# Performance work log

Hardware: AMD Instinct MI355X
Metric: run time of the kernel (lower is better)

Reference implementation:

```python
import jax, jax.numpy as jnp
import numpy as np

B, S, D = 8, 2048, 512


def setup_inputs() -> dict:
    key = jax.random.key(0)
    ks = jax.random.split(key, 11)
    scale = 1.0 / np.sqrt(D)
    inp = {"x": jax.random.normal(ks[0], (B, S, D), dtype=jnp.float32)}
    names = ["q", "k", "v", "g", "o"]
    for i, n in enumerate(names):
        inp[f"W{n}"] = jax.random.normal(ks[1 + 2 * i], (D, D), dtype=jnp.float32) * scale
        inp[f"b{n}"] = jax.random.normal(ks[2 + 2 * i], (D,), dtype=jnp.float32) * 0.01
    return inp


def reference(x, Wq, bq, Wk, bk, Wv, bv, Wg, bg, Wo, bo):
    # Projections (torch nn.Linear: x @ W.T + b)
    Q = x @ Wq.T + bq            # (B,S,D)
    K = x @ Wk.T + bk
    V = x @ Wv.T + bv
    gamma = jax.nn.sigmoid(x @ Wg.T + bg)

    # Recurrent linear-attention scan over time.
    # State St: (B,D,D); update: St = gamma_t[:, :, None] * St + k_t ⊗ v_t
    # (decay broadcasts along the key/row dimension, matching
    #  gamma_i.transpose(1,2) * S in the torch code)
    def step(St, qkvg):
        q_t, k_t, v_t, g_t = qkvg           # each (B,D)
        St = g_t[:, :, None] * St + k_t[:, :, None] * v_t[:, None, :]
        out_t = jnp.einsum('bd,bde->be', q_t, St)  # q_i @ S
        return St, out_t

    S0 = jnp.zeros((B, D, D), dtype=x.dtype)
    # time-major inputs for scan: (S,B,D)
    seq = (Q.transpose(1, 0, 2), K.transpose(1, 0, 2),
           V.transpose(1, 0, 2), gamma.transpose(1, 0, 2))
    _, outs = jax.lax.scan(step, S0, seq)   # outs: (S,B,D)
    O = outs.transpose(1, 0, 2)             # (B,S,D)
    return O @ Wo.T + bo
```

## Files before the change

### kernel.cpp

```cpp
#include <hip/hip_runtime.h>
#include <hip/hip_bf16.h>
#include <stdint.h>


#define B_ 8
#define S_ 2048
#define D_ 512
#define M_ (B_ * S_)
#define NSUB 64
#define SUBL 32
#define NSUP 8
#define SUPL 256

typedef __bf16 bf16x8 __attribute__((ext_vector_type(8)));
typedef float f32x4 __attribute__((ext_vector_type(4)));

__device__ __forceinline__ float bflo(uint32_t u){ return __uint_as_float(u<<16); }
__device__ __forceinline__ float bfhi(uint32_t u){ return __uint_as_float(u&0xffff0000u); }
__device__ __forceinline__ uint16_t f2bf(float f){
    uint32_t u = __float_as_uint(f);
    return (uint16_t)((u + 0x7fffu + ((u>>16)&1u)) >> 16);
}
__device__ __forceinline__ uint32_t pack2bf(float a, float b){
    return (uint32_t)f2bf(a) | ((uint32_t)f2bf(b)<<16);
}
__device__ __forceinline__ void gload16(const void* g, void* l){
    __builtin_amdgcn_global_load_lds(
        (const __attribute__((address_space(1))) uint32_t*)g,
        (__attribute__((address_space(3))) uint32_t*)l, 16, 0, 0);
}

__global__ __launch_bounds__(256) void conv_x(const float* __restrict__ in,
                                              uint16_t* __restrict__ out){
    const size_t i = ((size_t)blockIdx.x*256 + threadIdx.x)*8;
    float4 a = *(const float4*)&in[i];
    float4 b = *(const float4*)&in[i+4];
    uint4 o; o.x=pack2bf(a.x,a.y); o.y=pack2bf(a.z,a.w); o.z=pack2bf(b.x,b.y); o.w=pack2bf(b.z,b.w);
    *(uint4*)&out[i] = o;
}
__global__ __launch_bounds__(256) void conv_w(const float* w0, const float* w1, const float* w2,
                                              const float* w3, const float* w4,
                                              uint16_t* __restrict__ out){
    const float* ws[5] = {w0,w1,w2,w3,w4};
    const float* in = ws[blockIdx.y];
    uint16_t* o = out + (size_t)blockIdx.y*D_*D_;
    const size_t i = ((size_t)blockIdx.x*256 + threadIdx.x)*8;
    float4 a = *(const float4*)&in[i];
    float4 b = *(const float4*)&in[i+4];
    uint4 u; u.x=pack2bf(a.x,a.y); u.y=pack2bf(a.z,a.w); u.z=pack2bf(b.x,b.y); u.w=pack2bf(b.z,b.w);
    *(uint4*)&o[i] = u;
}

__global__ __launch_bounds__(256) void proj4(const uint16_t* __restrict__ A,
                                             const uint16_t* __restrict__ Wb,
                                             const float* __restrict__ bq_,
                                             const float* __restrict__ bk_,
                                             const float* __restrict__ bv_,
                                             const float* __restrict__ bg_,
                                             uint16_t* __restrict__ Qb,
                                             uint16_t* __restrict__ Kb,
                                             uint16_t* __restrict__ VT,
                                             uint16_t* __restrict__ Gb)
{
    __shared__ __attribute__((aligned(16))) uint16_t SM[2][16384];
    const int tid = threadIdx.x, wave = tid>>6, lane = tid&63;
    const int m0 = blockIdx.x*128, n0 = blockIdx.y*128;
    const int wr = (wave>>1)*64, wc = (wave&1)*64;
    const int fr = lane&15, fq = lane>>4;
    const int sect = blockIdx.y >> 2;
    const int n0c = n0 & 511;
    f32x4 acc[4][4] = {};

    auto STAGE = [&](int kt, int p){
        const int k0 = kt*64;
#pragma unroll
        for (int i = 0; i < 4; ++i) {
            const int c = i*256 + tid;
            const int row = c>>3, kc = ((c&7) ^ (row&7))*8;
            const int ldsb = (i*256 + wave*64)*8;
            gload16(&A [(size_t)(m0+row)*D_ + k0 + kc], &SM[p][ldsb]);
            gload16(&Wb[(size_t)(n0+row)*D_ + k0 + kc], &SM[p][8192+ldsb]);
        }
    };
    auto COMP = [&](int p){
#pragma unroll
        for (int kk = 0; kk < 64; kk += 32) {
            const int sc = (kk + fq*8) ^ ((fr&7)<<3);
            bf16x8 af[4], bfv[4];
#pragma unroll
            for (int m = 0; m < 4; ++m) af[m]  = *(const bf16x8*)&SM[p][(wr+m*16+fr)*64 + sc];
#pragma unroll
            for (int n = 0; n < 4; ++n) bfv[n] = *(const bf16x8*)&SM[p][8192+(wc+n*16+fr)*64 + sc];
            if (sect == 2) {
#pragma unroll
                for (int m = 0; m < 4; ++m)
#pragma unroll
                    for (int n = 0; n < 4; ++n)
                        acc[m][n] = __builtin_amdgcn_mfma_f32_16x16x32_bf16(bfv[n], af[m], acc[m][n], 0,0,0);
            } else {
#pragma unroll
                for (int m = 0; m < 4; ++m)
#pragma unroll
                    for (int n = 0; n < 4; ++n)
                        acc[m][n] = __builtin_amdgcn_mfma_f32_16x16x32_bf16(af[m], bfv[n], acc[m][n], 0,0,0);
            }
        }
    };

    STAGE(0, 0);
    __syncthreads();
    int p = 0;
    for (int kt = 0; kt < 8; ++kt) {
        if (kt < 7) STAGE(kt+1, p^1);
        COMP(p);
        __syncthreads();
        p ^= 1;
    }

    uint16_t (*L)[136] = (uint16_t(*)[136])&SM[0][0];
    const float* bias = (sect==0) ? bq_ : (sect==1) ? bk_ : (sect==2) ? bv_ : bg_;
    if (sect == 2) {
#pragma unroll
        for (int n = 0; n < 4; ++n)
#pragma unroll
            for (int q = 0; q < 4; ++q) {
                const int dvl = wc + n*16 + fq*4 + q;
                const float bvv = bias[n0c + dvl];
#pragma unroll
                for (int m = 0; m < 4; ++m)
                    L[dvl][wr + m*16 + fr] = f2bf(acc[m][n][q] + bvv);
            }
    } else {
#pragma unroll
        for (int n = 0; n < 4; ++n) {
            const int cl = wc + n*16 + fr;
            const float bvv = bias[n0c + cl];
#pragma unroll
            for (int m = 0; m < 4; ++m)
#pragma unroll
                for (int q = 0; q < 4; ++q) {
                    float c = acc[m][n][q] + bvv;
                    if (sect == 3) c = 1.f/(1.f + expf(-c));
                    L[wr + m*16 + fq*4 + q][cl] = f2bf(c);
                }
        }
    }
    __syncthreads();
    const int bb = m0 >> 11, t0 = m0 & 2047;
#pragma unroll
    for (int it = 0; it < 8; ++it) {
        const int r = it*16 + (tid>>4), c8 = (tid&15)*8;
        uint4 v = *(uint4*)&L[r][c8];
        if (sect == 0)      *(uint4*)&Qb[(size_t)(m0+r)*D_ + n0c + c8] = v;
        else if (sect == 1) *(uint4*)&Kb[(size_t)(m0+r)*D_ + n0c + c8] = v;
        else if (sect == 3) *(uint4*)&Gb[(size_t)(m0+r)*D_ + n0c + c8] = v;
        else                *(uint4*)&VT[((size_t)bb*D_ + n0c + r)*S_ + t0 + c8] = v;
    }
}

__global__ __launch_bounds__(256) void mfma_gemm(const uint16_t* __restrict__ A,
                                                 const uint16_t* __restrict__ Wt,
                                                 const float* __restrict__ bias,
                                                 float* __restrict__ out)
{
    __shared__ __attribute__((aligned(16))) uint16_t SM[2][16384];
    const int tid = threadIdx.x, wave = tid>>6, lane = tid&63;
    const int m0 = blockIdx.x*128, n0 = blockIdx.y*128;
    const int wr = (wave>>1)*64, wc = (wave&1)*64;
    const int fr = lane&15, fq = lane>>4;
    f32x4 acc[4][4] = {};

    auto STAGE = [&](int kt, int p){
        const int k0 = kt*64;
#pragma unroll
        for (int i = 0; i < 4; ++i) {
            const int c = i*256 + tid;
            const int row = c>>3, kc = ((c&7) ^ (row&7))*8;
            const int ldsb = (i*256 + wave*64)*8;
            gload16(&A [(size_t)(m0+row)*D_ + k0 + kc], &SM[p][ldsb]);
            gload16(&Wt[(size_t)(n0+row)*D_ + k0 + kc], &SM[p][8192+ldsb]);
        }
    };
    auto COMP = [&](int p){
#pragma unroll
        for (int kk = 0; kk < 64; kk += 32) {
            const int sc = (kk + fq*8) ^ ((fr&7)<<3);
            bf16x8 af[4], bfv[4];
#pragma unroll
            for (int m = 0; m < 4; ++m) af[m]  = *(const bf16x8*)&SM[p][(wr+m*16+fr)*64 + sc];
#pragma unroll
            for (int n = 0; n < 4; ++n) bfv[n] = *(const bf16x8*)&SM[p][8192+(wc+n*16+fr)*64 + sc];
#pragma unroll
            for (int m = 0; m < 4; ++m)
#pragma unroll
                for (int n = 0; n < 4; ++n)
                    acc[m][n] = __builtin_amdgcn_mfma_f32_16x16x32_bf16(af[m], bfv[n], acc[m][n], 0,0,0);
        }
    };

    STAGE(0, 0);
    __syncthreads();
    int p = 0;
    for (int kt = 0; kt < 8; ++kt) {
        if (kt < 7) STAGE(kt+1, p^1);
        COMP(p);
        __syncthreads();
        p ^= 1;
    }

    float (*L32)[68] = (float(*)[68])&SM[0][0];
#pragma unroll
    for (int h = 0; h < 2; ++h) {
        if (wc == h*64) {
#pragma unroll
            for (int n = 0; n < 4; ++n) {
                const float bvv = bias[n0 + wc + n*16 + fr];
#pragma unroll
                for (int m = 0; m < 4; ++m)
#pragma unroll
                    for (int q = 0; q < 4; ++q)
                        L32[wr + m*16 + fq*4 + q][n*16 + fr] = acc[m][n][q] + bvv;
            }
        }
        __syncthreads();
#pragma unroll
        for (int it = 0; it < 8; ++it) {
            const int r = it*16 + (tid>>4), c4 = (tid&15)*4;
            *(uint4*)&out[(size_t)(m0+r)*D_ + n0 + h*64 + c4] = *(uint4*)&L32[r][c4];
        }
        __syncthreads();
    }
}

__global__ __launch_bounds__(256) void prep(const uint16_t* __restrict__ Gb,
                                            uint16_t* __restrict__ Qb,
                                            uint16_t* __restrict__ Kb,
                                            uint16_t* __restrict__ KT,
                                            float* __restrict__ T)
{
    const int sub = blockIdx.x, b = blockIdx.y;
    const int tid = threadIdx.x;
    const int dk0 = tid*2;
    const size_t rowbase = ((size_t)b*S_ + sub*SUBL)*D_;
    const uint16_t* gp = Gb + rowbase + dk0;
    uint16_t*       qp = Qb + rowbase + dk0;
    uint16_t*       kp = Kb + rowbase + dk0;

    float mu0 = 1.f, mu1 = 1.f;
    uint32_t ksave[SUBL];
#pragma unroll
    for (int t = 0; t < SUBL; ++t) {
        const uint32_t g2 = *(const uint32_t*)(gp + (size_t)t*D_);
        const uint32_t qu = *(const uint32_t*)(qp + (size_t)t*D_);
        const uint32_t ku = *(const uint32_t*)(kp + (size_t)t*D_);
        mu0 = fmaxf(mu0*bflo(g2), 1e-30f);
        mu1 = fmaxf(mu1*bfhi(g2), 1e-30f);
        const float r0 = __builtin_amdgcn_rcpf(mu0);
        const float r1 = __builtin_amdgcn_rcpf(mu1);
        *(uint32_t*)(qp + (size_t)t*D_) = pack2bf(bflo(qu)*mu0, bfhi(qu)*mu1);
        const uint32_t kw = pack2bf(bflo(ku)*r0, bfhi(ku)*r1);
        *(uint32_t*)(kp + (size_t)t*D_) = kw;
        ksave[t] = kw;
    }
    T[((size_t)b*NSUB + sub)*D_ + dk0]     = mu0;
    T[((size_t)b*NSUB + sub)*D_ + dk0 + 1] = mu1;

    uint16_t* d0 = &KT[((size_t)b*D_ + dk0)*S_ + sub*SUBL];
    uint16_t* d1 = d0 + S_;
#pragma unroll
    for (int q4 = 0; q4 < 4; ++q4) {
        uint4 lo, hi;
        lo.x = (ksave[q4*8+0]&0xffffu) | (ksave[q4*8+1]<<16);
        lo.y = (ksave[q4*8+2]&0xffffu) | (ksave[q4*8+3]<<16);
        lo.z = (ksave[q4*8+4]&0xffffu) | (ksave[q4*8+5]<<16);
        lo.w = (ksave[q4*8+6]&0xffffu) | (ksave[q4*8+7]<<16);
        hi.x = (ksave[q4*8+0]>>16) | (ksave[q4*8+1]&0xffff0000u);
        hi.y = (ksave[q4*8+2]>>16) | (ksave[q4*8+3]&0xffff0000u);
        hi.z = (ksave[q4*8+4]>>16) | (ksave[q4*8+5]&0xffff0000u);
        hi.w = (ksave[q4*8+6]>>16) | (ksave[q4*8+7]&0xffff0000u);
        *(uint4*)&d0[q4*8] = lo;
        *(uint4*)&d1[q4*8] = hi;
    }
}

__global__ __launch_bounds__(512) void tables(const float* __restrict__ T,
                                              float* __restrict__ Pre,
                                              float* __restrict__ Suf,
                                              float* __restrict__ Lam)
{
    const int sp = blockIdx.x, b = blockIdx.y, dk = threadIdx.x;
    float run = 1.f;
#pragma unroll
    for (int m = 0; m < 8; ++m) {
        Pre[((size_t)b*NSUB + sp*8+m)*D_ + dk] = run;
        run *= T[((size_t)b*NSUB + sp*8+m)*D_ + dk];
    }
    Lam[((size_t)b*NSUP + sp)*D_ + dk] = run;
    float rs = 1.f;
#pragma unroll
    for (int m = 7; m >= 0; --m) {
        rs *= T[((size_t)b*NSUB + sp*8+m)*D_ + dk];
        Suf[((size_t)b*NSUB + sp*8+m)*D_ + dk] = rs;
    }
}

__device__ __forceinline__ int swz(int r, int c){ return r*D_ + (c ^ ((r&7)<<3)); }

__global__ __launch_bounds__(256) void pairsA(const uint16_t* __restrict__ Qt,
                                              const uint16_t* __restrict__ Kh,
                                              const float* __restrict__ T,
                                              uint16_t* __restrict__ P)
{
    __shared__ __attribute__((aligned(16))) uint16_t qs[SUBL*D_];
    __shared__ __attribute__((aligned(16))) uint16_t ks[SUBL*D_];
    __shared__ float D_lds[D_];
    const int idx = blockIdx.x, sp = blockIdx.y, b = blockIdx.z;
    int i = 0;
    while (((i+1)*(i+2))/2 <= idx) ++i;
    const int j = idx - (i*(i+1))/2;

    const int tid = threadIdx.x, wave = tid>>6, lane = tid&63;
    const int fr = lane&15, fq = lane>>4;
    const int mq = wave>>1, nq = wave&1;
    const size_t qrow = (size_t)b*S_ + sp*SUPL + i*SUBL;
    const size_t krow = (size_t)b*S_ + sp*SUPL + j*SUBL;
    const size_t prow = ((size_t)(b*NSUP + sp)*SUPL + i*SUBL);

#pragma unroll
    for (int z = 0; z < 8; ++z) {
        int ch = z*256 + tid, r = ch>>6, c = (ch&63)*8;
        *(uint4*)&qs[swz(r,c)] = *(const uint4*)&Qt[(qrow + r)*D_ + c];
    }
    const int dkA = tid*2, dkB = tid*2+1;
    float d0 = 1.f, d1 = 1.f;
    for (int m = j; m < i; ++m) {
        d0 *= T[((size_t)b*NSUB + sp*8 + m)*D_ + dkA];
        d1 *= T[((size_t)b*NSUB + sp*8 + m)*D_ + dkB];
    }
    D_lds[dkA] = d0; D_lds[dkB] = d1;
    __syncthreads();

#pragma unroll
    for (int z = 0; z < 8; ++z) {
        int ch = z*256 + tid, r = ch>>6, c = (ch&63)*8;
        uint4 u = *(const uint4*)&Kh[(krow + r)*D_ + c];
        uint4 o;
        o.x = pack2bf(bflo(u.x)*D_lds[c+0], bfhi(u.x)*D_lds[c+1]);
        o.y = pack2bf(bflo(u.y)*D_lds[c+2], bfhi(u.y)*D_lds[c+3]);
        o.z = pack2bf(bflo(u.z)*D_lds[c+4], bfhi(u.z)*D_lds[c+5]);
        o.w = pack2bf(bflo(u.w)*D_lds[c+6], bfhi(u.w)*D_lds[c+7]);
        *(uint4*)&ks[swz(r,c)] = o;
    }
    __syncthreads();

    f32x4 a0 = {}, a1 = {}, a2 = {}, a3 = {};
#pragma unroll
    for (int kk = 0; kk < 512; kk += 128) {
        bf16x8 q0 = *(const bf16x8*)&qs[swz(mq*16+fr, kk      + fq*8)];
        bf16x8 k0 = *(const bf16x8*)&ks[swz(nq*16+fr, kk      + fq*8)];
        bf16x8 q1 = *(const bf16x8*)&qs[swz(mq*16+fr, kk + 32 + fq*8)];
        bf16x8 k1 = *(const bf16x8*)&ks[swz(nq*16+fr, kk + 32 + fq*8)];
        bf16x8 q2 = *(const bf16x8*)&qs[swz(mq*16+fr, kk + 64 + fq*8)];
        bf16x8 k2 = *(const bf16x8*)&ks[swz(nq*16+fr, kk + 64 + fq*8)];
        bf16x8 q3 = *(const bf16x8*)&qs[swz(mq*16+fr, kk + 96 + fq*8)];
        bf16x8 k3 = *(const bf16x8*)&ks[swz(nq*16+fr, kk + 96 + fq*8)];
        a0 = __builtin_amdgcn_mfma_f32_16x16x32_bf16(q0, k0, a0, 0,0,0);
        a1 = __builtin_amdgcn_mfma_f32_16x16x32_bf16(q1, k1, a1, 0,0,0);
        a2 = __builtin_amdgcn_mfma_f32_16x16x32_bf16(q2, k2, a2, 0,0,0);
        a3 = __builtin_amdgcn_mfma_f32_16x16x32_bf16(q3, k3, a3, 0,0,0);
    }
    const int ul = nq*16 + fr;
#pragma unroll
    for (int q_ = 0; q_ < 4; ++q_) {
        const int tl = mq*16 + fq*4 + q_;
        float v = a0[q_] + a1[q_] + a2[q_] + a3[q_];
        if (i == j && ul > tl) v = 0.f;
        P[(prow + tl)*SUPL + j*SUBL + ul] = f2bf(v);
    }
}

__global__ __launch_bounds__(256) void dsgemm(const uint16_t* __restrict__ VT,
                                              const uint16_t* __restrict__ KT,
                                              const float* __restrict__ Suf,
                                              uint16_t* __restrict__ Sst)
{
    __shared__ __attribute__((aligned(16))) uint16_t As[2][128][40];
    __shared__ __attribute__((aligned(16))) uint16_t Bs[2][128][40];
    const int tile = blockIdx.x, c = blockIdx.y, b = blockIdx.z;
    const int m0 = (tile&3)*128, n0 = (tile>>2)*128;
    const int tid = threadIdx.x, wave = tid>>6, lane = tid&63;
    const int wr = (wave>>1)*64, wc = (wave&1)*64;
    const int fr = lane&15, fq = lane>>4;
    f32x4 acc[4][4] = {};

    auto STAGE = [&](int j, int p){
        const int t0 = c*SUPL + j*SUBL;
#pragma unroll
        for (int ch = tid; ch < 512; ch += 256) {
            int row = ch>>2, tc = (ch&3)*8;
            *(uint4*)&As[p][row][tc] = *(const uint4*)&VT[((size_t)b*D_ + m0+row)*S_ + t0 + tc];
        }
#pragma unroll
        for (int ch = tid; ch < 512; ch += 256) {
            int row = ch>>2, tc = (ch&3)*8;
            uint4 u = *(const uint4*)&KT[((size_t)b*D_ + n0+row)*S_ + t0 + tc];
            float sf = Suf[((size_t)b*NSUB + c*8 + j)*D_ + n0 + row];
            uint4 o;
            o.x = pack2bf(bflo(u.x)*sf, bfhi(u.x)*sf);
            o.y = pack2bf(bflo(u.y)*sf, bfhi(u.y)*sf);
            o.z = pack2bf(bflo(u.z)*sf, bfhi(u.z)*sf);
            o.w = pack2bf(bflo(u.w)*sf, bfhi(u.w)*sf);
            *(uint4*)&Bs[p][row][tc] = o;
        }
    };

    STAGE(0, 0);
    __syncthreads();
    int p = 0;
    for (int j = 0; j < 8; ++j) {
        if (j < 7) STAGE(j+1, p^1);
        bf16x8 af[4], bf[4];
#pragma unroll
        for (int m = 0; m < 4; ++m) af[m] = *(const bf16x8*)&As[p][wr+m*16+fr][fq*8];
#pragma unroll
        for (int n = 0; n < 4; ++n) bf[n] = *(const bf16x8*)&Bs[p][wc+n*16+fr][fq*8];
#pragma unroll
        for (int m = 0; m < 4; ++m)
#pragma unroll
            for (int n = 0; n < 4; ++n)
                acc[m][n] = __builtin_amdgcn_mfma_f32_16x16x32_bf16(af[m], bf[n], acc[m][n], 0,0,0);
        __syncthreads();
        p ^= 1;
    }
#pragma unroll
    for (int n = 0; n < 4; ++n) {
        const int dk = n0 + wc + n*16 + fr;
#pragma unroll
        for (int m = 0; m < 4; ++m)
#pragma unroll
            for (int q = 0; q < 4; ++q) {
                const int dv = m0 + wr + m*16 + fq*4 + q;
                Sst[(((size_t)c*B_ + b)*D_ + dv)*D_ + dk] = f2bf(acc[m][n][q]);
            }
    }
}

__global__ __launch_bounds__(256) void scanfix(uint16_t* __restrict__ Sst,
                                               const float* __restrict__ Lam)
{
    const int id = blockIdx.x*256 + threadIdx.x;
    const int g = id & 63, dv = (id>>6) & 511, b = id >> 15;
    const int dk = g*8;
    float s[8];
    {
        uint4 u = *(const uint4*)&Sst[(((size_t)0*B_ + b)*D_ + dv)*D_ + dk];
        s[0]=bflo(u.x); s[1]=bfhi(u.x); s[2]=bflo(u.y); s[3]=bfhi(u.y);
        s[4]=bflo(u.z); s[5]=bfhi(u.z); s[6]=bflo(u.w); s[7]=bfhi(u.w);
    }
    for (int c = 1; c < 7; ++c) {
        const size_t bs = (((size_t)c*B_ + b)*D_ + dv)*D_ + dk;
        uint4 d = *(const uint4*)&Sst[bs];
        float4 l0 = *(const float4*)&Lam[((size_t)b*NSUP + c)*D_ + dk];
        float4 l1 = *(const float4*)&Lam[((size_t)b*NSUP + c)*D_ + dk + 4];
        s[0] = l0.x*s[0] + bflo(d.x); s[1] = l0.y*s[1] + bfhi(d.x);
        s[2] = l0.z*s[2] + bflo(d.y); s[3] = l0.w*s[3] + bfhi(d.y);
        s[4] = l1.x*s[4] + bflo(d.z); s[5] = l1.y*s[5] + bfhi(d.z);
        s[6] = l1.z*s[6] + bflo(d.w); s[7] = l1.w*s[7] + bfhi(d.w);
        uint4 o;
        o.x = pack2bf(s[0],s[1]); o.y = pack2bf(s[2],s[3]);
        o.z = pack2bf(s[4],s[5]); o.w = pack2bf(s[6],s[7]);
        *(uint4*)&Sst[bs] = o;
    }
}

__global__ __launch_bounds__(256) void bigout(const uint16_t* __restrict__ Qt,
                                              const float* __restrict__ Pre,
                                              const uint16_t* __restrict__ Sst,
                                              const uint16_t* __restrict__ Pb,
                                              const uint16_t* __restrict__ VT,
                                              uint16_t* __restrict__ O)
{
    __shared__ __attribute__((aligned(16))) uint16_t SM[2][16384];
    __shared__ float PreL[4*512];
    const int m0 = blockIdx.x*128, n0 = blockIdx.y*128;
    const int b = blockIdx.z>>3, sp = blockIdx.z&7;
    const int tid = threadIdx.x, wave = tid>>6, lane = tid&63;
    const int wr = (wave>>1)*64, wc = (wave&1)*64;
    const int fr = lane&15, fq = lane>>4;
    const int i0 = m0>>5;

#pragma unroll
    for (int z = 0; z < 8; ++z) {
        int idx = z*256 + tid;
        PreL[idx] = Pre[((size_t)b*NSUB + sp*8 + i0 + (idx>>9))*D_ + (idx&511)];
    }
    f32x4 acc[4][4] = {};
    uint4 areg[4];

    auto ISSUE_A = [&](int kt){
        const int k0 = kt*64;
#pragma unroll
        for (int z = 0; z < 4; ++z) {
            int ch = z*256 + tid, r = ch>>3, cc = (ch&7)*8;
            areg[z] = *(const uint4*)&Qt[((size_t)b*S_ + sp*SUPL + m0 + r)*D_ + k0 + cc];
        }
    };
    auto WRITE_A = [&](int kt, int p){
        const int k0 = kt*64;
#pragma unroll
        for (int z = 0; z < 4; ++z) {
            int ch = z*256 + tid, r = ch>>3, cc = (ch&7)*8;
            const float* pr = &PreL[((r>>5)<<9) + k0 + cc];
            uint4 u = areg[z];
            uint4 o;
            o.x = pack2bf(bflo(u.x)*pr[0], bfhi(u.x)*pr[1]);
            o.y = pack2bf(bflo(u.y)*pr[2], bfhi(u.y)*pr[3]);
            o.z = pack2bf(bflo(u.z)*pr[4], bfhi(u.z)*pr[5]);
            o.w = pack2bf(bflo(u.w)*pr[6], bfhi(u.w)*pr[7]);
            *(uint4*)&SM[p][r*64 + (cc ^ ((r&7)<<3))] = o;
        }
    };
    auto STAGE_A_GL = [&](int kt, int p){
        const int u0 = (kt-8)*64;
#pragma unroll
        for (int z = 0; z < 4; ++z) {
            int ch = z*256 + tid, row = ch>>3, kc = ((ch&7) ^ (row&7))*8;
            int ldsb = (z*256 + wave*64)*8;
            gload16(&Pb[((size_t)(b*NSUP + sp)*SUPL + m0 + row)*SUPL + u0 + kc], &SM[p][ldsb]);
        }
    };
    auto STAGE_B = [&](int kt, int p){
        if (kt < 8) {
            const int k0 = kt*64;
#pragma unroll
            for (int z = 0; z < 4; ++z) {
                int ch = z*256 + tid, row = ch>>3, kc = ((ch&7) ^ (row&7))*8;
                int ldsb = (z*256 + wave*64)*8;
                gload16(&Sst[(((size_t)(sp-1)*B_ + b)*D_ + n0 + row)*D_ + k0 + kc], &SM[p][8192+ldsb]);
            }
        } else {
            const int u0 = (kt-8)*64;
#pragma unroll
            for (int z = 0; z < 4; ++z) {
                int ch = z*256 + tid, row = ch>>3, kc = ((ch&7) ^ (row&7))*8;
                int ldsb = (z*256 + wave*64)*8;
                gload16(&VT[((size_t)b*D_ + n0 + row)*S_ + sp*SUPL + u0 + kc], &SM[p][8192+ldsb]);
            }
        }
    };
    auto COMP = [&](int p, int kt){
        const bf16x8 zz = {};
#pragma unroll
        for (int kk = 0; kk < 64; kk += 32) {
            const int sc = (kk + fq*8) ^ ((fr&7)<<3);
            bf16x8 af[4], bfv[4];
#pragma unroll
            for (int m = 0; m < 4; ++m) af[m] = *(const bf16x8*)&SM[p][(wr+m*16+fr)*64 + sc];
            if (kt >= 8) {
                const int jb = ((kt-8)*64 + kk) >> 5;
#pragma unroll
                for (int m = 0; m < 4; ++m) {
                    const int ib = (m0 + wr + m*16) >> 5;
                    if (jb > ib) af[m] = zz;
                }
            }
#pragma unroll
            for (int n = 0; n < 4; ++n) bfv[n] = *(const bf16x8*)&SM[p][8192+(wc+n*16+fr)*64 + sc];
#pragma unroll
            for (int m = 0; m < 4; ++m)
#pragma unroll
                for (int n = 0; n < 4; ++n)
                    acc[m][n] = __builtin_amdgcn_mfma_f32_16x16x32_bf16(af[m], bfv[n], acc[m][n], 0,0,0);
        }
    };

    const int kt0 = (sp == 0) ? 8 : 0;
    if (kt0 < 8) {
        ISSUE_A(kt0);
        STAGE_B(kt0, 0);
        __syncthreads();
        WRITE_A(kt0, 0);
    } else {
        STAGE_A_GL(kt0, 0);
        STAGE_B(kt0, 0);
    }
    __syncthreads();

    int p = 0;
    for (int kt = kt0; kt < 12; ++kt) {
        const int nxt = kt + 1;
        if (nxt < 12) {
            if (nxt < 8) ISSUE_A(nxt); else STAGE_A_GL(nxt, p^1);
            STAGE_B(nxt, p^1);
        }
        COMP(p, kt);
        if (nxt < 12 && nxt < 8) WRITE_A(nxt, p^1);
        __syncthreads();
        p ^= 1;
    }

    uint16_t (*L)[136] = (uint16_t(*)[136])&SM[0][0];
#pragma unroll
    for (int n = 0; n < 4; ++n) {
        const int cl = wc + n*16 + fr;
#pragma unroll
        for (int m = 0; m < 4; ++m)
#pragma unroll
            for (int q = 0; q < 4; ++q)
                L[wr + m*16 + fq*4 + q][cl] = f2bf(acc[m][n][q]);
    }
    __syncthreads();
#pragma unroll
    for (int it = 0; it < 8; ++it) {
        const int r = it*16 + (tid>>4), c8 = (tid&15)*8;
        *(uint4*)&O[((size_t)b*S_ + sp*SUPL + m0 + r)*D_ + n0 + c8] = *(uint4*)&L[r][c8];
    }
}

extern "C" void kernel_launch(void* const* d_in, const int* in_sizes, int n_in,
                              void* d_out, int out_size, void* d_ws, size_t ws_size,
                              hipStream_t stream)
{
    (void)in_sizes; (void)n_in; (void)out_size; (void)ws_size;
    const float* x  = (const float*)d_in[0];
    const float* Wq = (const float*)d_in[1];  const float* bq = (const float*)d_in[2];
    const float* Wk = (const float*)d_in[3];  const float* bk = (const float*)d_in[4];
    const float* Wv = (const float*)d_in[5];  const float* bv = (const float*)d_in[6];
    const float* Wg = (const float*)d_in[7];  const float* bg = (const float*)d_in[8];
    const float* Wo = (const float*)d_in[9];  const float* bo = (const float*)d_in[10];

    char* w = (char*)d_ws;
    const size_t MD2 = (size_t)M_*D_*2;
    uint16_t* Wb = (uint16_t*)w;                       w += 5*(size_t)D_*D_*2;
    uint16_t* xb = (uint16_t*)w;                       w += MD2;
    uint16_t* Qb = (uint16_t*)w;                       w += MD2;
    uint16_t* Kb = (uint16_t*)w;                       w += MD2;
    uint16_t* KT = (uint16_t*)w;                       w += MD2;
    uint16_t* VT = (uint16_t*)w;                       w += MD2;
    uint16_t* Gb = (uint16_t*)w;                       w += MD2;
    uint16_t* Sst = (uint16_t*)w;                      w += (size_t)7*B_*D_*D_*2;
    uint16_t* Pb  = (uint16_t*)w;                      w += (size_t)B_*NSUP*SUPL*SUPL*2;
    float*    T   = (float*)w;                         w += (size_t)B_*NSUB*D_*4;
    float*    Pre = (float*)w;                         w += (size_t)B_*NSUB*D_*4;
    float*    Suf = (float*)w;                         w += (size_t)B_*NSUB*D_*4;
    float*    Lam = (float*)w;                         w += (size_t)B_*NSUP*D_*4;

    conv_x<<<dim3(M_*D_/2048), 256, 0, stream>>>(x, xb);
    conv_w<<<dim3(D_*D_/2048, 5), 256, 0, stream>>>(Wq, Wk, Wv, Wg, Wo, Wb);

    proj4<<<dim3(M_/128, 16), 256, 0, stream>>>(xb, Wb, bq, bk, bv, bg, Qb, Kb, VT, Gb);

    prep<<<dim3(NSUB, B_), 256, 0, stream>>>(Gb, Qb, Kb, KT, T);
    tables<<<dim3(NSUP, B_), 512, 0, stream>>>(T, Pre, Suf, Lam);

    pairsA<<<dim3(36, NSUP, B_), 256, 0, stream>>>(Qb, Kb, T, Pb);
    dsgemm<<<dim3(16, 7, B_), 256, 0, stream>>>(VT, KT, Suf, Sst);
    scanfix<<<dim3(1024), 256, 0, stream>>>(Sst, Lam);

    bigout<<<dim3(2, 4, B_*NSUP), 256, 0, stream>>>(Qb, Pre, Sst, Pb, VT, xb);

    mfma_gemm<<<dim3(M_/128, D_/128), 256, 0, stream>>>(xb, Wb + 4*(size_t)D_*D_, bo, (float*)d_out);
}
```

Before: 201.9 us.

## Retile projection GEMM to 256x256 blocks with 4-stage pipeline and swizzled grid

The fused Q/K/V/G projection kernel moves from 128x128 tiles with double buffering to 256x256 tiles on 512 threads. It uses a 4-deep LDS pipeline with explicit vmcnt waits, raised wave priority during MFMA work, and a half-by-half epilogue. The output GEMM also gets a 1D grid with a block swizzle for better L2 locality. Larger tiles and deeper prefetch aim to raise arithmetic intensity and hide load latency, at the cost of higher register and LDS pressure, which may lower occupancy.

```diff
diff --git a/kernel.cpp b/kernel.cpp
--- a/kernel.cpp
+++ b/kernel.cpp
@@ -51,110 +51,140 @@
     *(uint4*)&o[i] = u;
 }
 
-__global__ __launch_bounds__(256) void proj4(const uint16_t* __restrict__ A,
-                                             const uint16_t* __restrict__ Wb,
-                                             const float* __restrict__ bq_,
-                                             const float* __restrict__ bk_,
-                                             const float* __restrict__ bv_,
-                                             const float* __restrict__ bg_,
-                                             uint16_t* __restrict__ Qb,
-                                             uint16_t* __restrict__ Kb,
-                                             uint16_t* __restrict__ VT,
-                                             uint16_t* __restrict__ Gb)
-{
-    __shared__ __attribute__((aligned(16))) uint16_t SM[2][16384];
+__global__ __launch_bounds__(512, 2) void proj4(const uint16_t* __restrict__ A,
+                                                const uint16_t* __restrict__ Wb,
+                                                const float* __restrict__ bq_,
+                                                const float* __restrict__ bk_,
+                                                const float* __restrict__ bv_,
+                                                const float* __restrict__ bg_,
+                                                uint16_t* __restrict__ Qb,
+                                                uint16_t* __restrict__ Kb,
+                                                uint16_t* __restrict__ VT,
+                                                uint16_t* __restrict__ Gb)
+{
+    __shared__ __attribute__((aligned(16))) uint16_t SM[65536];
+    const int id  = blockIdx.x;
+    const int bx  = id & 63, by = id >> 6;
     const int tid = threadIdx.x, wave = tid>>6, lane = tid&63;
-    const int m0 = blockIdx.x*128, n0 = blockIdx.y*128;
-    const int wr = (wave>>1)*64, wc = (wave&1)*64;
-    const int fr = lane&15, fq = lane>>4;
-    const int sect = blockIdx.y >> 2;
-    const int n0c = n0 & 511;
-    f32x4 acc[4][4] = {};
-
-    auto STAGE = [&](int kt, int p){
-        const int k0 = kt*64;
-#pragma unroll
-        for (int i = 0; i < 4; ++i) {
-            const int c = i*256 + tid;
-            const int row = c>>3, kc = ((c&7) ^ (row&7))*8;
-            const int ldsb = (i*256 + wave*64)*8;
-            gload16(&A [(size_t)(m0+row)*D_ + k0 + kc], &SM[p][ldsb]);
-            gload16(&Wb[(size_t)(n0+row)*D_ + k0 + kc], &SM[p][8192+ldsb]);
-        }
-    };
-    auto COMP = [&](int p){
-#pragma unroll
-        for (int kk = 0; kk < 64; kk += 32) {
-            const int sc = (kk + fq*8) ^ ((fr&7)<<3);
-            bf16x8 af[4], bfv[4];
-#pragma unroll
-            for (int m = 0; m < 4; ++m) af[m]  = *(const bf16x8*)&SM[p][(wr+m*16+fr)*64 + sc];
-#pragma unroll
-            for (int n = 0; n < 4; ++n) bfv[n] = *(const bf16x8*)&SM[p][8192+(wc+n*16+fr)*64 + sc];
-            if (sect == 2) {
-#pragma unroll
-                for (int m = 0; m < 4; ++m)
-#pragma unroll
-                    for (int n = 0; n < 4; ++n)
-                        acc[m][n] = __builtin_amdgcn_mfma_f32_16x16x32_bf16(bfv[n], af[m], acc[m][n], 0,0,0);
-            } else {
-#pragma unroll
-                for (int m = 0; m < 4; ++m)
-#pragma unroll
-                    for (int n = 0; n < 4; ++n)
-                        acc[m][n] = __builtin_amdgcn_mfma_f32_16x16x32_bf16(af[m], bfv[n], acc[m][n], 0,0,0);
-            }
-        }
-    };
-
-    STAGE(0, 0);
-    __syncthreads();
-    int p = 0;
-    for (int kt = 0; kt < 8; ++kt) {
-        if (kt < 7) STAGE(kt+1, p^1);
-        COMP(p);
-        __syncthreads();
-        p ^= 1;
-    }
-
-    uint16_t (*L)[136] = (uint16_t(*)[136])&SM[0][0];
+    const int m0  = bx*256, n0 = by*256;
+    const int wm  = wave>>2, wn = wave&3;
+    const int fr  = lane&15, fq = lane>>4;
+    const int sect = by >> 1;
+    const int n0c  = (by&1)*256;
+    const int sx   = (fr ^ (fr>>2)) & 3;
+    const int col  = (fq ^ sx) * 8;
+
+    f32x4 acc[8][4] = {};
+
+    auto STAGE = [&](int ct, int s){
+        const int base = s*16384;
+#pragma unroll
+        for (int z = 0; z < 2; ++z) {
+            const int ch  = z*512 + tid;
+            const int row = ch >> 2, sl = ch & 3;
+            const int kc  = (sl ^ ((row ^ (row>>2)) & 3)) * 8;
+            const int ldsb = base + (z*512 + wave*64)*8;
+            gload16(&A [(size_t)(m0+row)*D_ + ct*32 + kc], &SM[ldsb]);
+            gload16(&Wb[(size_t)(n0+row)*D_ + ct*32 + kc], &SM[ldsb + 8192]);
+        }
+    };
+
+    STAGE(0, 0); STAGE(1, 1); STAGE(2, 2);
+#pragma unroll
+    for (int i = 0; i < 16; ++i) {
+        const int s = i & 3;
+        if (i < 13) STAGE(i+3, (i+3)&3);
+        __builtin_amdgcn_sched_barrier(0);
+        if      (i < 13) asm volatile("s_waitcnt vmcnt(12)" ::: "memory");
+        else if (i == 13) asm volatile("s_waitcnt vmcnt(8)"  ::: "memory");
+        else if (i == 14) asm volatile("s_waitcnt vmcnt(4)"  ::: "memory");
+        else              asm volatile("s_waitcnt vmcnt(0)"  ::: "memory");
+        __builtin_amdgcn_s_barrier();
+        __builtin_amdgcn_sched_barrier(0);
+
+        const int ab = s*16384;
+        bf16x8 af[8], bfv[4];
+#pragma unroll
+        for (int mf = 0; mf < 8; ++mf)
+            af[mf] = *(const bf16x8*)&SM[ab + (wm*128 + mf*16 + fr)*32 + col];
+#pragma unroll
+        for (int nf = 0; nf < 4; ++nf)
+            bfv[nf] = *(const bf16x8*)&SM[ab + 8192 + (wn*64 + nf*16 + fr)*32 + col];
+
+        __builtin_amdgcn_s_setprio(1);
+        if (sect == 2) {
+#pragma unroll
+            for (int nf = 0; nf < 4; ++nf)
+#pragma unroll
+                for (int mf = 0; mf < 8; ++mf)
+                    acc[mf][nf] = __builtin_amdgcn_mfma_f32_16x16x32_bf16(bfv[nf], af[mf], acc[mf][nf], 0,0,0);
+        } else {
+#pragma unroll
+            for (int nf = 0; nf < 4; ++nf)
+#pragma unroll
+                for (int mf = 0; mf < 8; ++mf)
+                    acc[mf][nf] = __builtin_amdgcn_mfma_f32_16x16x32_bf16(af[mf], bfv[nf], acc[mf][nf], 0,0,0);
+        }
+        __builtin_amdgcn_s_setprio(0);
+        __builtin_amdgcn_sched_barrier(0);
+        __builtin_amdgcn_s_barrier();
+        __builtin_amdgcn_sched_barrier(0);
+    }
+
     const float* bias = (sect==0) ? bq_ : (sect==1) ? bk_ : (sect==2) ? bv_ : bg_;
     if (sect == 2) {
-#pragma unroll
-        for (int n = 0; n < 4; ++n)
-#pragma unroll
-            for (int q = 0; q < 4; ++q) {
-                const int dvl = wc + n*16 + fq*4 + q;
-                const float bvv = bias[n0c + dvl];
-#pragma unroll
-                for (int m = 0; m < 4; ++m)
-                    L[dvl][wr + m*16 + fr] = f2bf(acc[m][n][q] + bvv);
+        uint16_t (*Lv)[132] = (uint16_t(*)[132])SM;
+        const int bb = m0 >> 11, t0 = m0 & 2047;
+#pragma unroll
+        for (int h = 0; h < 2; ++h) {
+            if (wm == h) {
+#pragma unroll
+                for (int nf = 0; nf < 4; ++nf)
+#pragma unroll
+                    for (int q = 0; q < 4; ++q) {
+                        const int dv = wn*64 + nf*16 + fq*4 + q;
+                        const float bvv = bias[n0c + dv];
+#pragma unroll
+                        for (int mf = 0; mf < 8; ++mf)
+                            Lv[dv][mf*16 + fr] = f2bf(acc[mf][nf][q] + bvv);
+                    }
             }
+            __syncthreads();
+            const int r = tid>>1, c0 = (tid&1)*64;
+#pragma unroll
+            for (int e = 0; e < 8; ++e)
+                *(uint4*)&VT[((size_t)bb*D_ + n0c + r)*S_ + t0 + h*128 + c0 + e*8] =
+                    *(uint4*)&Lv[r][c0 + e*8];
+            __syncthreads();
+        }
     } else {
-#pragma unroll
-        for (int n = 0; n < 4; ++n) {
-            const int cl = wc + n*16 + fr;
-            const float bvv = bias[n0c + cl];
-#pragma unroll
-            for (int m = 0; m < 4; ++m)
-#pragma unroll
-                for (int q = 0; q < 4; ++q) {
-                    float c = acc[m][n][q] + bvv;
-                    if (sect == 3) c = 1.f/(1.f + expf(-c));
-                    L[wr + m*16 + fq*4 + q][cl] = f2bf(c);
+        uint16_t (*L)[264] = (uint16_t(*)[264])SM;
+        uint16_t* dst = (sect==0) ? Qb : (sect==1) ? Kb : Gb;
+#pragma unroll
+        for (int h = 0; h < 2; ++h) {
+            if (wm == h) {
+#pragma unroll
+                for (int nf = 0; nf < 4; ++nf) {
+                    const int cl = wn*64 + nf*16 + fr;
+                    const float bvv = bias[n0c + cl];
+#pragma unroll
+                    for (int mf = 0; mf < 8; ++mf)
+#pragma unroll
+                        for (int q = 0; q < 4; ++q) {
+                            float c = acc[mf][nf][q] + bvv;
+                            if (sect == 3) c = 1.f/(1.f + expf(-c));
+                            L[mf*16 + fq*4 + q][cl] = f2bf(c);
+                        }
                 }
-        }
-    }
-    __syncthreads();
-    const int bb = m0 >> 11, t0 = m0 & 2047;
-#pragma unroll
-    for (int it = 0; it < 8; ++it) {
-        const int r = it*16 + (tid>>4), c8 = (tid&15)*8;
-        uint4 v = *(uint4*)&L[r][c8];
-        if (sect == 0)      *(uint4*)&Qb[(size_t)(m0+r)*D_ + n0c + c8] = v;
-        else if (sect == 1) *(uint4*)&Kb[(size_t)(m0+r)*D_ + n0c + c8] = v;
-        else if (sect == 3) *(uint4*)&Gb[(size_t)(m0+r)*D_ + n0c + c8] = v;
-        else                *(uint4*)&VT[((size_t)bb*D_ + n0c + r)*S_ + t0 + c8] = v;
+            }
+            __syncthreads();
+            const int r = tid>>2, c0 = (tid&3)*64;
+#pragma unroll
+            for (int e = 0; e < 8; ++e)
+                *(uint4*)&dst[(size_t)(m0 + h*128 + r)*D_ + n0c + c0 + e*8] =
+                    *(uint4*)&L[r][c0 + e*8];
+            __syncthreads();
+        }
     }
 }
 
@@ -164,8 +194,11 @@
                                                  float* __restrict__ out)
 {
     __shared__ __attribute__((aligned(16))) uint16_t SM[2][16384];
+    const int id = blockIdx.x;
+    const int bx = (id & 7) + 8*((id >> 3) & 15);
+    const int by = id >> 7;
     const int tid = threadIdx.x, wave = tid>>6, lane = tid&63;
-    const int m0 = blockIdx.x*128, n0 = blockIdx.y*128;
+    const int m0 = bx*128, n0 = by*128;
     const int wr = (wave>>1)*64, wc = (wave&1)*64;
     const int fr = lane&15, fq = lane>>4;
     f32x4 acc[4][4] = {};
@@ -648,7 +681,7 @@
     conv_x<<<dim3(M_*D_/2048), 256, 0, stream>>>(x, xb);
     conv_w<<<dim3(D_*D_/2048, 5), 256, 0, stream>>>(Wq, Wk, Wv, Wg, Wo, Wb);
 
-    proj4<<<dim3(M_/128, 16), 256, 0, stream>>>(xb, Wb, bq, bk, bv, bg, Qb, Kb, VT, Gb);
+    proj4<<<dim3(512), 512, 0, stream>>>(xb, Wb, bq, bk, bv, bg, Qb, Kb, VT, Gb);
 
     prep<<<dim3(NSUB, B_), 256, 0, stream>>>(Gb, Qb, Kb, KT, T);
     tables<<<dim3(NSUP, B_), 512, 0, stream>>>(T, Pre, Suf, Lam);
@@ -659,5 +692,5 @@
 
     bigout<<<dim3(2, 4, B_*NSUP), 256, 0, stream>>>(Qb, Pre, Sst, Pb, VT, xb);
 
-    mfma_gemm<<<dim3(M_/128, D_/128), 256, 0, stream>>>(xb, Wb + 4*(size_t)D_*D_, bo, (float*)d_out);
-}
+    mfma_gemm<<<dim3(512), 256, 0, stream>>>(xb, Wb + 4*(size_t)D_*D_, bo, (float*)d_out);
+}
```

After: 424.3 us. +110.1%, slower.

## Fuse x fp32-to-bf16 conversion into projection GEMM and remap block order

Applied to the files above, without the earlier changes.

Removes the separate conv_x kernel. proj4 now loads fp32 x directly into registers, converts it to bf16 and writes it into swizzled LDS, overlapping the next tile's global loads with the current MFMA compute. Both GEMMs switch to a 1D grid with a grouped block-index remap so that consecutive blocks share row tiles, aiming at better cache reuse. The fused path reads x in fp32 once per column tile (16 times) instead of reading bf16 copies, which adds global traffic and register pressure in exchange for dropping a full pass over x.

```diff
diff --git a/kernel.cpp b/kernel.cpp
--- a/kernel.cpp
+++ b/kernel.cpp
@@ -30,14 +30,6 @@
         (__attribute__((address_space(3))) uint32_t*)l, 16, 0, 0);
 }
 
-__global__ __launch_bounds__(256) void conv_x(const float* __restrict__ in,
-                                              uint16_t* __restrict__ out){
-    const size_t i = ((size_t)blockIdx.x*256 + threadIdx.x)*8;
-    float4 a = *(const float4*)&in[i];
-    float4 b = *(const float4*)&in[i+4];
-    uint4 o; o.x=pack2bf(a.x,a.y); o.y=pack2bf(a.z,a.w); o.z=pack2bf(b.x,b.y); o.w=pack2bf(b.z,b.w);
-    *(uint4*)&out[i] = o;
-}
 __global__ __launch_bounds__(256) void conv_w(const float* w0, const float* w1, const float* w2,
                                               const float* w3, const float* w4,
                                               uint16_t* __restrict__ out){
@@ -51,7 +43,7 @@
     *(uint4*)&o[i] = u;
 }
 
-__global__ __launch_bounds__(256) void proj4(const uint16_t* __restrict__ A,
+__global__ __launch_bounds__(256) void proj4(const float* __restrict__ X,
                                              const uint16_t* __restrict__ Wb,
                                              const float* __restrict__ bq_,
                                              const float* __restrict__ bk_,
@@ -63,22 +55,47 @@
                                              uint16_t* __restrict__ Gb)
 {
     __shared__ __attribute__((aligned(16))) uint16_t SM[2][16384];
+    const int id = blockIdx.x;
+    const int bx = (id & 7) + 8*((id >> 3) & 15);
+    const int by = id >> 7;
     const int tid = threadIdx.x, wave = tid>>6, lane = tid&63;
-    const int m0 = blockIdx.x*128, n0 = blockIdx.y*128;
+    const int m0 = bx*128, n0 = by*128;
     const int wr = (wave>>1)*64, wc = (wave&1)*64;
     const int fr = lane&15, fq = lane>>4;
-    const int sect = blockIdx.y >> 2;
+    const int sect = by >> 2;
     const int n0c = n0 & 511;
     f32x4 acc[4][4] = {};
-
-    auto STAGE = [&](int kt, int p){
+    float4 areg[4][2];
+
+    auto ISSUE_A = [&](int kt){
+        const int k0 = kt*64;
+#pragma unroll
+        for (int z = 0; z < 4; ++z) {
+            const int c = z*256 + tid, row = c>>3, cc = (c&7)*8;
+            const float* src = &X[(size_t)(m0+row)*D_ + k0 + cc];
+            areg[z][0] = *(const float4*)src;
+            areg[z][1] = *(const float4*)(src + 4);
+        }
+    };
+    auto WRITE_A = [&](int p){
+#pragma unroll
+        for (int z = 0; z < 4; ++z) {
+            const int c = z*256 + tid, row = c>>3, cc = (c&7)*8;
+            uint4 o;
+            o.x = pack2bf(areg[z][0].x, areg[z][0].y);
+            o.y = pack2bf(areg[z][0].z, areg[z][0].w);
+            o.z = pack2bf(areg[z][1].x, areg[z][1].y);
+            o.w = pack2bf(areg[z][1].z, areg[z][1].w);
+            *(uint4*)&SM[p][row*64 + (cc ^ ((row&7)<<3))] = o;
+        }
+    };
+    auto STAGE_B = [&](int kt, int p){
         const int k0 = kt*64;
 #pragma unroll
         for (int i = 0; i < 4; ++i) {
             const int c = i*256 + tid;
             const int row = c>>3, kc = ((c&7) ^ (row&7))*8;
             const int ldsb = (i*256 + wave*64)*8;
-            gload16(&A [(size_t)(m0+row)*D_ + k0 + kc], &SM[p][ldsb]);
             gload16(&Wb[(size_t)(n0+row)*D_ + k0 + kc], &SM[p][8192+ldsb]);
         }
     };
@@ -107,12 +124,14 @@
         }
     };
 
-    STAGE(0, 0);
+    ISSUE_A(0); STAGE_B(0, 0); WRITE_A(0);
     __syncthreads();
     int p = 0;
     for (int kt = 0; kt < 8; ++kt) {
-        if (kt < 7) STAGE(kt+1, p^1);
+        const int nxt = kt + 1;
+        if (nxt < 8) { ISSUE_A(nxt); STAGE_B(nxt, p^1); }
         COMP(p);
+        if (nxt < 8) WRITE_A(p^1);
         __syncthreads();
         p ^= 1;
     }
@@ -164,8 +183,11 @@
                                                  float* __restrict__ out)
 {
     __shared__ __attribute__((aligned(16))) uint16_t SM[2][16384];
+    const int id = blockIdx.x;
+    const int bx = (id & 7) + 8*((id >> 3) & 15);
+    const int by = id >> 7;
     const int tid = threadIdx.x, wave = tid>>6, lane = tid&63;
-    const int m0 = blockIdx.x*128, n0 = blockIdx.y*128;
+    const int m0 = bx*128, n0 = by*128;
     const int wr = (wave>>1)*64, wc = (wave&1)*64;
     const int fr = lane&15, fq = lane>>4;
     f32x4 acc[4][4] = {};
@@ -632,7 +654,7 @@
     char* w = (char*)d_ws;
     const size_t MD2 = (size_t)M_*D_*2;
     uint16_t* Wb = (uint16_t*)w;                       w += 5*(size_t)D_*D_*2;
-    uint16_t* xb = (uint16_t*)w;                       w += MD2;
+    uint16_t* Ob = (uint16_t*)w;                       w += MD2;
     uint16_t* Qb = (uint16_t*)w;                       w += MD2;
     uint16_t* Kb = (uint16_t*)w;                       w += MD2;
     uint16_t* KT = (uint16_t*)w;                       w += MD2;
@@ -645,10 +667,9 @@
     float*    Suf = (float*)w;                         w += (size_t)B_*NSUB*D_*4;
     float*    Lam = (float*)w;                         w += (size_t)B_*NSUP*D_*4;
 
-    conv_x<<<dim3(M_*D_/2048), 256, 0, stream>>>(x, xb);
     conv_w<<<dim3(D_*D_/2048, 5), 256, 0, stream>>>(Wq, Wk, Wv, Wg, Wo, Wb);
 
-    proj4<<<dim3(M_/128, 16), 256, 0, stream>>>(xb, Wb, bq, bk, bv, bg, Qb, Kb, VT, Gb);
+    proj4<<<dim3(2048), 256, 0, stream>>>(x, Wb, bq, bk, bv, bg, Qb, Kb, VT, Gb);
 
     prep<<<dim3(NSUB, B_), 256, 0, stream>>>(Gb, Qb, Kb, KT, T);
     tables<<<dim3(NSUP, B_), 512, 0, stream>>>(T, Pre, Suf, Lam);
@@ -657,7 +678,7 @@
     dsgemm<<<dim3(16, 7, B_), 256, 0, stream>>>(VT, KT, Suf, Sst);
     scanfix<<<dim3(1024), 256, 0, stream>>>(Sst, Lam);
 
-    bigout<<<dim3(2, 4, B_*NSUP), 256, 0, stream>>>(Qb, Pre, Sst, Pb, VT, xb);
-
-    mfma_gemm<<<dim3(M_/128, D_/128), 256, 0, stream>>>(xb, Wb + 4*(size_t)D_*D_, bo, (float*)d_out);
-}
+    bigout<<<dim3(2, 4, B_*NSUP), 256, 0, stream>>>(Qb, Pre, Sst, Pb, VT, Ob);
+
+    mfma_gemm<<<dim3(512), 256, 0, stream>>>(Ob, Wb + 4*(size_t)D_*D_, bo, (float*)d_out);
+}
```

New measurement: 215.3 us. 6.6% more time.
